# Performance work log

Measured on AMD Instinct MI355X. Metric: run time of the kernel, lower is better.

The kernel has to match this reference:

```python
import jax, jax.numpy as jnp
import numpy as np

CROP = 48
THRESHOLD = 0.5
IOU_THRESHOLD = 0.5


def _conv(x, w, b):
    # x: [N,H,W,C], w: [kh,kw,Cin,Cout]
    y = jax.lax.conv_general_dilated(x, w, (1, 1), 'VALID',
                                     dimension_numbers=('NHWC', 'HWIO', 'NHWC'))
    return y + b


def _prelu(x, a):
    # a broadcasts over the channel-last axis
    return jnp.where(x >= 0, x, a * x)


def _maxpool(x, k, s, p):
    return jax.lax.reduce_window(x, -jnp.inf, jax.lax.max,
                                 (1, k, k, 1), (1, s, s, 1),
                                 ((0, 0), (p, p), (p, p), (0, 0)))


def _nms_keep(boxes, scores, valid, iou_thr):
    # fixed-shape greedy NMS (torchvision semantics: suppress iou > thr)
    N = boxes.shape[0]
    s = jnp.where(valid, scores, -jnp.inf)
    order = jnp.argsort(-s)
    b = boxes[order]
    x1, y1, x2, y2 = b[:, 0], b[:, 1], b[:, 2], b[:, 3]
    area = (x2 - x1) * (y2 - y1)
    xx1 = jnp.maximum(x1[:, None], x1[None, :])
    yy1 = jnp.maximum(y1[:, None], y1[None, :])
    xx2 = jnp.minimum(x2[:, None], x2[None, :])
    yy2 = jnp.minimum(y2[:, None], y2[None, :])
    inter = jnp.clip(xx2 - xx1, 0.0) * jnp.clip(yy2 - yy1, 0.0)
    iou = inter / (area[:, None] + area[None, :] - inter + 1e-12)
    keep0 = valid[order]
    idx = jnp.arange(N)

    def body(i, keep):
        sup = (iou[i] > iou_thr) & (idx > i) & keep[i] & keep
        return keep & ~sup

    keep_sorted = jax.lax.fori_loop(0, N, body, keep0)
    return jnp.zeros(N, bool).at[order].set(keep_sorted)


def setup_inputs() -> dict:
    key = jax.random.key(0)
    ks = jax.random.split(key, 24)
    H = W = 1024
    N = 2048
    image = jax.random.uniform(ks[0], (H, W, 3), jnp.float32) * 255.0
    x1 = jax.random.uniform(ks[1], (N,), jnp.float32) * (W - 130)
    y1 = jax.random.uniform(ks[2], (N,), jnp.float32) * (H - 130)
    bw = 20.0 + jax.random.uniform(ks[3], (N,), jnp.float32) * 100.0
    bh = 20.0 + jax.random.uniform(ks[4], (N,), jnp.float32) * 100.0
    bboxes = jnp.stack([x1, y1, x1 + bw, y1 + bh], axis=1)
    rn = lambda k, sh, s: jax.random.normal(k, sh, jnp.float32) * s
    return {
        'bboxes': bboxes, 'image': image,
        'conv1_w': rn(ks[5], (3, 3, 3, 32), 0.05), 'conv1_b': rn(ks[6], (32,), 0.01),
        'prelu1': 0.25 * jnp.ones((32,), jnp.float32),
        'conv2_w': rn(ks[7], (3, 3, 32, 64), 0.05), 'conv2_b': rn(ks[8], (64,), 0.01),
        'prelu2': 0.25 * jnp.ones((64,), jnp.float32),
        'conv3_w': rn(ks[9], (3, 3, 64, 64), 0.05), 'conv3_b': rn(ks[10], (64,), 0.01),
        'prelu3': 0.25 * jnp.ones((64,), jnp.float32),
        'conv4_w': rn(ks[11], (2, 2, 64, 128), 0.05), 'conv4_b': rn(ks[12], (128,), 0.01),
        'prelu4': 0.25 * jnp.ones((128,), jnp.float32),
        'fc5_w': rn(ks[13], (256, 1152), 0.02), 'fc5_b': rn(ks[14], (256,), 0.01),
        'prelu5': 0.25 * jnp.ones((256,), jnp.float32),
        'fc6a_w': rn(ks[15], (2, 256), 0.1), 'fc6a_b': rn(ks[16], (2,), 0.01),
        'fc6b_w': rn(ks[17], (4, 256), 0.1), 'fc6b_b': rn(ks[18], (4,), 0.01),
    }


def reference(bboxes, image, conv1_w, conv1_b, prelu1, conv2_w, conv2_b, prelu2,
              conv3_w, conv3_b, prelu3, conv4_w, conv4_b, prelu4,
              fc5_w, fc5_b, prelu5, fc6a_w, fc6a_b, fc6b_w, fc6b_b):
    H, W = image.shape[0], image.shape[1]
    N = bboxes.shape[0]
    # preprocess (torch: (x - 127.5) * 0.0078125)
    data = (image - 127.5) * 0.0078125  # [H,W,3]
    # clip boxes in place like the torch forward
    bx1 = jnp.clip(bboxes[:, 0], 0.0, None)
    by1 = jnp.clip(bboxes[:, 1], 0.0, None)
    bx2 = jnp.clip(bboxes[:, 2], None, float(W))
    by2 = jnp.clip(bboxes[:, 3], None, float(H))
    bb = jnp.stack([bx1, by1, bx2, by2], axis=1)  # clipped boxes [N,4]
    # integer crop windows (torch .int() truncation; coords >= 0)
    ib = bb.astype(jnp.int32)
    cw = jnp.maximum(ib[:, 2] - ib[:, 0], 1)
    ch = jnp.maximum(ib[:, 3] - ib[:, 1], 1)
    # nearest-neighbor resize to 48x48 (F.interpolate default mode='nearest')
    r = jnp.arange(CROP, dtype=jnp.int32)
    xs = ib[:, 0:1] + (r[None, :] * cw[:, None]) // CROP  # [N,48]
    ys = ib[:, 1:2] + (r[None, :] * ch[:, None]) // CROP  # [N,48]
    crops = data[ys[:, :, None], xs[:, None, :], :]  # [N,48,48,3] gather
    # CNN trunk
    h = _maxpool(_prelu(_conv(crops, conv1_w, conv1_b), prelu1), 3, 2, 1)
    h = _maxpool(_prelu(_conv(h, conv2_w, conv2_b), prelu2), 3, 2, 0)
    h = _maxpool(_prelu(_conv(h, conv3_w, conv3_b), prelu3), 2, 2, 0)
    h = _prelu(_conv(h, conv4_w, conv4_b), prelu4)  # [N,3,3,128]
    h = jnp.transpose(h, (0, 3, 1, 2)).reshape(N, -1)  # NCHW flatten like torch -> [N,1152]
    h = _prelu(h @ fc5_w.T + fc5_b, prelu5)  # [N,256]
    cls = jax.nn.softmax(h @ fc6a_w.T + fc6a_b, axis=1)  # [N,2]
    reg = h @ fc6b_w.T + fc6b_b  # [N,4]
    score = cls[:, 1]
    valid = score >= THRESHOLD
    w = bb[:, 2] - bb[:, 0]
    hgt = bb[:, 3] - bb[:, 1]
    out = jnp.stack([bb[:, 0] + reg[:, 0] * w,
                     bb[:, 1] + reg[:, 1] * hgt,
                     bb[:, 2] + reg[:, 2] * w,
                     bb[:, 3] + reg[:, 3] * hgt], axis=1)  # [N,4]
    keep = _nms_keep(out, score, valid, IOU_THRESHOLD)
    return jnp.where(keep[:, None], out, 0.0)
```

## Files before the change

kernel.cpp:

```cpp
#include <hip/hip_runtime.h>
#include <math.h>
#include <stdint.h>

#define NBOX 2048

#define P1_RS 25
#define P1_CS 576
#define P1_SZ 18432

__device__ __forceinline__ void fma4(float4& a, float s, const float4& w) {
  a.x = fmaf(s, w.x, a.x); a.y = fmaf(s, w.y, a.y);
  a.z = fmaf(s, w.z, a.z); a.w = fmaf(s, w.w, a.w);
}
__device__ __forceinline__ float4 max4(float4 a, float4 b) {
  return make_float4(fmaxf(a.x,b.x), fmaxf(a.y,b.y), fmaxf(a.z,b.z), fmaxf(a.w,b.w));
}
__device__ __forceinline__ float4 max34(float4 a, float4 b, float4 c) {
  return max4(max4(a, b), c);
}
__device__ __forceinline__ float4 prelu4(float4 v, float4 a) {
  float4 r;
  r.x = v.x >= 0.f ? v.x : a.x*v.x;
  r.y = v.y >= 0.f ? v.y : a.y*v.y;
  r.z = v.z >= 0.f ? v.z : a.z*v.z;
  r.w = v.w >= 0.f ? v.w : a.w*v.w;
  return r;
}
__device__ __forceinline__ float4 shfl4(float4 v, int src) {
  float4 r;
  r.x = __shfl(v.x, src, 64); r.y = __shfl(v.y, src, 64);
  r.z = __shfl(v.z, src, 64); r.w = __shfl(v.w, src, 64);
  return r;
}

__global__ __launch_bounds__(256) void k1_crop_conv1(
    const float* __restrict__ bboxes, const float* __restrict__ image,
    const float* __restrict__ w1, const float* __restrict__ b1, const float* __restrict__ a1,
    float* __restrict__ p1ws, int box0)
{
  __shared__ float crop[48*48*3];
  __shared__ float w1s[27*32];
  __shared__ float b1s[32], a1s[32];
  const int tid = threadIdx.x;
  const int n = box0 + blockIdx.x;

  for (int idx = tid; idx < 27*32; idx += 256) w1s[idx] = w1[idx];
  if (tid < 32) { b1s[tid] = b1[tid]; a1s[tid] = a1[tid]; }

  float f0 = bboxes[n*4+0], f1 = bboxes[n*4+1], f2 = bboxes[n*4+2], f3 = bboxes[n*4+3];
  float bx1 = fmaxf(f0, 0.f), by1 = fmaxf(f1, 0.f);
  float bx2 = fminf(f2, 1024.f), by2 = fminf(f3, 1024.f);
  int ix1 = (int)bx1, iy1 = (int)by1, ix2 = (int)bx2, iy2 = (int)by2;
  int cw = ix2 - ix1; if (cw < 1) cw = 1;
  int ch = iy2 - iy1; if (ch < 1) ch = 1;

  for (int idx = tid; idx < 6912; idx += 256) {
    int c = idx % 3; int t = idx / 3; int j = t % 48; int i = t / 48;
    int gx = ix1 + (j * cw) / 48;
    int gy = iy1 + (i * ch) / 48;
    float v = image[(gy*1024 + gx)*3 + c];
    crop[idx] = (v - 127.5f) * 0.0078125f;
  }
  __syncthreads();

  float* p1o = p1ws + (size_t)blockIdx.x * P1_SZ;

  for (int slot = tid; slot < 1104; slot += 256) {
    int cq = slot & 7;
    int t2 = slot >> 3;
    int pjq = t2 % 6;
    int pi  = t2 / 6;
    int pj0 = pjq * 4;
    int c0 = 2*pj0 - 1;
    float4 bias  = *(const float4*)&b1s[cq*4];
    float4 alpha = *(const float4*)&a1s[cq*4];
    float4 mx[4];
#pragma unroll
    for (int t = 0; t < 4; t++) mx[t] = make_float4(-3.0e38f,-3.0e38f,-3.0e38f,-3.0e38f);

#pragma unroll
    for (int dr = 0; dr < 3; dr++) {
      int r = 2*pi - 1 + dr;
      if (r < 0 || r > 45) continue;
      float4 acc[9];
#pragma unroll
      for (int c = 0; c < 9; c++) acc[c] = bias;
#pragma unroll
      for (int kh = 0; kh < 3; kh++) {
        int row = r + kh;
        float s[33];
#pragma unroll
        for (int d = 0; d < 11; d++) {
          int cc = c0 + d; cc = cc < 0 ? 0 : (cc > 47 ? 47 : cc);
          int base = row*144 + cc*3;
          s[d*3+0] = crop[base+0];
          s[d*3+1] = crop[base+1];
          s[d*3+2] = crop[base+2];
        }
#pragma unroll
        for (int kw = 0; kw < 3; kw++) {
#pragma unroll
          for (int ci = 0; ci < 3; ci++) {
            float4 w = *(const float4*)&w1s[((kh*3+kw)*3+ci)*32 + cq*4];
#pragma unroll
            for (int c = 0; c < 9; c++) fma4(acc[c], s[(c+kw)*3+ci], w);
          }
        }
      }
#pragma unroll
      for (int c = 0; c < 9; c++) {
        int cabs = c0 + c;
        if (cabs < 0 || cabs > 45) continue;
        float4 pv = prelu4(acc[c], alpha);
#pragma unroll
        for (int t = 0; t < 4; t++) {
          if (c >= 2*t && c <= 2*t+2) mx[t] = max4(mx[t], pv);
        }
      }
    }
#pragma unroll
    for (int t = 0; t < 4; t++) {
      int pj = pj0 + t;
      if (pj < 23) {
        int base = pi*P1_RS + pj;
        p1o[(cq*4+0)*P1_CS + base] = mx[t].x;
        p1o[(cq*4+1)*P1_CS + base] = mx[t].y;
        p1o[(cq*4+2)*P1_CS + base] = mx[t].z;
        p1o[(cq*4+3)*P1_CS + base] = mx[t].w;
      }
    }
  }
}

#define K2_LOADW(W, CI, KH) { \
  const float* wp_ = w2 + (((KH)*3)*32 + (CI))*64 + co0; \
  W[0] = *(const float4*)(wp_);            W[1] = *(const float4*)(wp_ + 4); \
  W[2] = *(const float4*)(wp_ + 2048);     W[3] = *(const float4*)(wp_ + 2052); \
  W[4] = *(const float4*)(wp_ + 4096);     W[5] = *(const float4*)(wp_ + 4100); }

#define K2_COMP(W, CI, KH) { \
  const float* ip_ = &in_s[(CI)*P1_CS + (rl+(KH))*P1_RS + j0]; \
  float s_[9]; \
  _Pragma("unroll") for (int d_ = 0; d_ < 9; d_++) s_[d_] = ip_[d_]; \
  _Pragma("unroll") for (int kw_ = 0; kw_ < 3; kw_++) { \
    _Pragma("unroll") for (int jj_ = 0; jj_ < 7; jj_++) { \
      fma4(acc[jj_][0], s_[jj_+kw_], W[kw_*2]); \
      fma4(acc[jj_][1], s_[jj_+kw_], W[kw_*2+1]); } } }

#define K2_STORE8(PJ, LO, HI) { \
  float* d_ = p2o + (size_t)co0*120 + pi*12 + (PJ); \
  float4 lo_ = (LO), hi_ = (HI); \
  d_[0]   = lo_.x; d_[120] = lo_.y; d_[240] = lo_.z; d_[360] = lo_.w; \
  d_[480] = hi_.x; d_[600] = hi_.y; d_[720] = hi_.z; d_[840] = hi_.w; }

__global__ __launch_bounds__(512, 4) void k2_conv2(
    const float* __restrict__ w2, const float* __restrict__ b2, const float* __restrict__ a2,
    const float* __restrict__ p1ws, float* __restrict__ p2ws)
{
  __shared__ float in_s[P1_SZ];
  const int tid = threadIdx.x;
  const float* p1o = p1ws + (size_t)blockIdx.x * P1_SZ;
  float* p2o = p2ws + (size_t)blockIdx.x * 7680;

  for (int i4 = tid; i4 < P1_SZ/4; i4 += 512)
    *(float4*)&in_s[i4*4] = *(const float4*)&p1o[i4*4];
  __syncthreads();

  const int wav = __builtin_amdgcn_readfirstlane(tid >> 6);
  const int lane = tid & 63;
  int jt = lane / 21;
  int rl = lane - jt * 21;
  if (lane == 63) { jt = 2; rl = 20; }
  const int j0 = jt * 7;
  const int co0 = wav * 8;

  float4 bL = *(const float4*)&b2[co0];
  float4 bH = *(const float4*)&b2[co0+4];
  float4 aL = *(const float4*)&a2[co0];
  float4 aH = *(const float4*)&a2[co0+4];

  float4 acc[7][2];
#pragma unroll
  for (int jj = 0; jj < 7; jj++) { acc[jj][0] = bL; acc[jj][1] = bH; }

  float4 wA[6], wB[6];
  K2_LOADW(wA, 0, 0);
#pragma unroll 1
  for (int ci = 0; ci < 32; ci += 2) {
    K2_LOADW(wB, ci, 1);
    K2_COMP(wA, ci, 0);
    K2_LOADW(wA, ci, 2);
    K2_COMP(wB, ci, 1);
    K2_LOADW(wB, ci+1, 0);
    K2_COMP(wA, ci, 2);
    K2_LOADW(wA, ci+1, 1);
    K2_COMP(wB, ci+1, 0);
    K2_LOADW(wB, ci+1, 2);
    K2_COMP(wA, ci+1, 1);
    if (ci + 2 < 32) K2_LOADW(wA, ci+2, 0);
    K2_COMP(wB, ci+1, 2);
  }

#pragma unroll
  for (int jj = 0; jj < 7; jj++) {
    acc[jj][0] = prelu4(acc[jj][0], aL);
    acc[jj][1] = prelu4(acc[jj][1], aH);
  }

#pragma unroll
  for (int jj = 0; jj < 7; jj++) {
#pragma unroll
    for (int h = 0; h < 2; h++) {
      float4 v = acc[jj][h];
      float4 d1 = shfl4(v, lane + 1);
      float4 d2 = shfl4(v, lane + 2);
      acc[jj][h] = max34(v, d1, d2);
    }
  }
  float4 r0[2], r1[2];
#pragma unroll
  for (int h = 0; h < 2; h++) {
    r0[h] = shfl4(acc[0][h], lane + 21);
    r1[h] = shfl4(acc[1][h], lane + 21);
  }

  if (((rl & 1) == 0) && rl <= 18) {
    const int pi = rl >> 1;
    if (jt == 0) {
      K2_STORE8(0, max34(acc[0][0],acc[1][0],acc[2][0]), max34(acc[0][1],acc[1][1],acc[2][1]));
      K2_STORE8(1, max34(acc[2][0],acc[3][0],acc[4][0]), max34(acc[2][1],acc[3][1],acc[4][1]));
      K2_STORE8(2, max34(acc[4][0],acc[5][0],acc[6][0]), max34(acc[4][1],acc[5][1],acc[6][1]));
      K2_STORE8(3, max34(acc[6][0],r0[0],r1[0]),          max34(acc[6][1],r0[1],r1[1]));
    } else if (jt == 1) {
      K2_STORE8(4, max34(acc[1][0],acc[2][0],acc[3][0]), max34(acc[1][1],acc[2][1],acc[3][1]));
      K2_STORE8(5, max34(acc[3][0],acc[4][0],acc[5][0]), max34(acc[3][1],acc[4][1],acc[5][1]));
      K2_STORE8(6, max34(acc[5][0],acc[6][0],r0[0]),     max34(acc[5][1],acc[6][1],r0[1]));
    } else {
      K2_STORE8(7, max34(acc[0][0],acc[1][0],acc[2][0]), max34(acc[0][1],acc[1][1],acc[2][1]));
      K2_STORE8(8, max34(acc[2][0],acc[3][0],acc[4][0]), max34(acc[2][1],acc[3][1],acc[4][1]));
      K2_STORE8(9, max34(acc[4][0],acc[5][0],acc[6][0]), max34(acc[4][1],acc[5][1],acc[6][1]));
    }
  }
}

#define K3_LOADW(W, CI, KH) { \
  const float* wp_ = w3 + (((KH)*3)*64 + (CI))*64 + co0; \
  W[0] = *(const float4*)(wp_);            W[1] = *(const float4*)(wp_ + 4); \
  W[2] = *(const float4*)(wp_ + 4096);     W[3] = *(const float4*)(wp_ + 4100); \
  W[4] = *(const float4*)(wp_ + 8192);     W[5] = *(const float4*)(wp_ + 8196); }

#define K3_COMP(W, CI, KH) { \
  const float* ip_ = ibase + (CI)*120 + (KH)*12; \
  float2 sA_ = *(const float2*)(ip_); \
  float2 sB_ = *(const float2*)(ip_ + 2); \
  float s_[4] = {sA_.x, sA_.y, sB_.x, sB_.y}; \
  _Pragma("unroll") for (int kw_ = 0; kw_ < 3; kw_++) { \
    _Pragma("unroll") for (int c_ = 0; c_ < 2; c_++) { \
      fma4(acc[c_][0], s_[c_+kw_], W[kw_*2]); \
      fma4(acc[c_][1], s_[c_+kw_], W[kw_*2+1]); } } }

__global__ __launch_bounds__(512, 4) void k3_conv3(
    const float* __restrict__ w3, const float* __restrict__ b3, const float* __restrict__ a3,
    const float* __restrict__ p2ws, float* __restrict__ p3ws)
{
  __shared__ float in_s[15376];
  const int tid = threadIdx.x;
  const float* p2o = p2ws + (size_t)(blockIdx.x*2) * 7680;
  float* p3o0 = p3ws + (size_t)(blockIdx.x*2) * 1024;

  for (int i4 = tid; i4 < 3840; i4 += 512) {
    int bb = (i4 >= 1920) ? 1 : 0;
    int k = i4 - bb*1920;
    *(float4*)&in_s[bb*7688 + k*4] = *(const float4*)&p2o[(size_t)bb*7680 + k*4];
  }
  __syncthreads();

  const int wav = __builtin_amdgcn_readfirstlane(tid >> 6);
  const int lane = tid & 63;
  const int b  = lane >> 5;
  const int r  = (lane >> 2) & 7;
  const int cg = lane & 3;
  const int co0 = wav * 8;

  float4 bL = *(const float4*)&b3[co0];
  float4 bH = *(const float4*)&b3[co0+4];
  float4 aL = *(const float4*)&a3[co0];
  float4 aH = *(const float4*)&a3[co0+4];

  float4 acc[2][2];
  acc[0][0] = bL; acc[0][1] = bH; acc[1][0] = bL; acc[1][1] = bH;

  const float* ibase = &in_s[b*7688 + r*12 + cg*2];

  float4 wA[6], wB[6];
  K3_LOADW(wA, 0, 0);
#pragma unroll 1
  for (int ci = 0; ci < 64; ci += 2) {
    K3_LOADW(wB, ci, 1);
    K3_COMP(wA, ci, 0);
    K3_LOADW(wA, ci, 2);
    K3_COMP(wB, ci, 1);
    K3_LOADW(wB, ci+1, 0);
    K3_COMP(wA, ci, 2);
    K3_LOADW(wA, ci+1, 1);
    K3_COMP(wB, ci+1, 0);
    K3_LOADW(wB, ci+1, 2);
    K3_COMP(wA, ci+1, 1);
    if (ci + 2 < 64) K3_LOADW(wA, ci+2, 0);
    K3_COMP(wB, ci+1, 2);
  }

  float4 hm[2];
#pragma unroll
  for (int h = 0; h < 2; h++) {
    float4 p0 = prelu4(acc[0][h], h ? aH : aL);
    float4 p1 = prelu4(acc[1][h], h ? aH : aL);
    hm[h] = max4(p0, p1);
  }
  float4 o[2];
#pragma unroll
  for (int h = 0; h < 2; h++) {
    float4 d = shfl4(hm[h], lane + 4);
    o[h] = max4(hm[h], d);
  }
  if ((r & 1) == 0) {
    const int pi = r >> 1;
    float* d = p3o0 + b*1024 + (size_t)co0*16 + pi*4 + cg;
    d[0]   = o[0].x; d[16]  = o[0].y; d[32]  = o[0].z; d[48]  = o[0].w;
    d[64]  = o[1].x; d[80]  = o[1].y; d[96]  = o[1].z; d[112] = o[1].w;
  }
}

__global__ __launch_bounds__(128) void k4_conv4(
    const float* __restrict__ w4, const float* __restrict__ b4, const float* __restrict__ a4,
    const float* __restrict__ p3ws, float* __restrict__ c4ws)
{
  __shared__ float p3s[1024];
  __shared__ float w4s[64*128];
  __shared__ float b4s[128], a4s[128];
  const int tid = threadIdx.x;
  const float* p3o = p3ws + (size_t)blockIdx.x * 1024;
  float* c4o = c4ws + (size_t)blockIdx.x * 1152;
  b4s[tid] = b4[tid]; a4s[tid] = a4[tid];
  for (int idx4 = tid; idx4 < 256; idx4 += 128)
    *(float4*)&p3s[idx4*4] = *(const float4*)&p3o[idx4*4];

  const int slot = tid;
  const bool active = slot < 96;
  const int cq = slot & 31, rl = slot >> 5;
  float4 acc[3];
  bool first = true;
  for (int cg = 0; cg < 4; cg++) {
    __syncthreads();
    for (int idx4 = tid; idx4 < 2048; idx4 += 128) {
      int co4 = idx4 & 31, kkcl = idx4 >> 5;
      int khkw = kkcl >> 4, cl = kkcl & 15;
      *(float4*)&w4s[kkcl*128 + co4*4] =
          *(const float4*)&w4[(khkw*64 + cg*16 + cl)*128 + co4*4];
    }
    __syncthreads();
    if (active) {
      if (first) {
        float4 b = *(const float4*)&b4s[cq*4];
        acc[0]=b; acc[1]=b; acc[2]=b; first=false;
      }
      for (int cl = 0; cl < 16; cl++) {
        int ci = cg*16 + cl;
#pragma unroll
        for (int kh = 0; kh < 2; kh++) {
          float4 sv = *(const float4*)&p3s[ci*16 + (rl+kh)*4];
          float s[4] = {sv.x, sv.y, sv.z, sv.w};
#pragma unroll
          for (int kw = 0; kw < 2; kw++) {
            float4 w = *(const float4*)&w4s[((kh*2+kw)*16+cl)*128 + cq*4];
#pragma unroll
            for (int v = 0; v < 3; v++) fma4(acc[v], s[v+kw], w);
          }
        }
      }
    }
  }
  if (active) {
    float4 alpha = *(const float4*)&a4s[cq*4];
#pragma unroll
    for (int v = 0; v < 3; v++) {
      float4 p = prelu4(acc[v], alpha);
      c4o[(cq*4+0)*9 + rl*3 + v] = p.x;
      c4o[(cq*4+1)*9 + rl*3 + v] = p.y;
      c4o[(cq*4+2)*9 + rl*3 + v] = p.z;
      c4o[(cq*4+3)*9 + rl*3 + v] = p.w;
    }
  }
}

__global__ __launch_bounds__(256) void k5_fc(
    const float* __restrict__ fc5w, const float* __restrict__ fc5b, const float* __restrict__ a5,
    const float* __restrict__ w6a, const float* __restrict__ b6a,
    const float* __restrict__ w6b, const float* __restrict__ b6b,
    const float* __restrict__ bboxes, const float* __restrict__ c4ws,
    float* __restrict__ ws_scores, float* __restrict__ ws_boxes, int box0)
{
  __shared__ float c4s[8*1152];
  __shared__ float hs[8*256];
  __shared__ float l6[8][6];
  __shared__ float b5s[256], a5s[256];
  const int tid = threadIdx.x;
  const int lb0 = blockIdx.x * 8;
  b5s[tid] = fc5b[tid]; a5s[tid] = a5[tid];
  for (int idx4 = tid; idx4 < 2304; idx4 += 256)
    *(float4*)&c4s[idx4*4] = *(const float4*)&c4ws[(size_t)lb0*1152 + idx4*4];
  __syncthreads();

  const int og = tid & 31, bl = tid >> 5;
  float acc[8] = {0,0,0,0,0,0,0,0};
  const float* cbase = &c4s[bl*1152];
  for (int k = 0; k < 1152; k += 4) {
    float4 a = *(const float4*)&cbase[k];
#pragma unroll
    for (int u = 0; u < 8; u++) {
      int o = og + 32*u;
      float4 w = *(const float4*)&fc5w[(size_t)o*1152 + k];
      acc[u] += a.x*w.x + a.y*w.y + a.z*w.z + a.w*w.w;
    }
  }
#pragma unroll
  for (int u = 0; u < 8; u++) {
    int o = og + 32*u;
    float h = acc[u] + b5s[o];
    h = h >= 0.f ? h : a5s[o]*h;
    hs[bl*256 + o] = h;
  }
  __syncthreads();
  if (tid < 48) {
    int b = tid / 6, oi = tid % 6;
    const float* w = (oi < 2) ? &w6a[oi*256] : &w6b[(oi-2)*256];
    float d = (oi < 2) ? b6a[oi] : b6b[oi-2];
    const float* hh = &hs[b*256];
    for (int k = 0; k < 256; k++) d += hh[k]*w[k];
    l6[b][oi] = d;
  }
  __syncthreads();
  if (tid < 8) {
    int n = box0 + lb0 + tid;
    float l0 = l6[tid][0], l1 = l6[tid][1];
    float m = fmaxf(l0, l1);
    float e0 = expf(l0-m), e1 = expf(l1-m);
    float score = e1/(e0+e1);
    float r0 = l6[tid][2], r1 = l6[tid][3], r2 = l6[tid][4], r3 = l6[tid][5];
    float f0 = bboxes[n*4+0], f1 = bboxes[n*4+1], f2 = bboxes[n*4+2], f3 = bboxes[n*4+3];
    float bx1 = fmaxf(f0, 0.f), by1 = fmaxf(f1, 0.f);
    float bx2 = fminf(f2, 1024.f), by2 = fminf(f3, 1024.f);
    float w_ = bx2-bx1, h_ = by2-by1;
    ws_scores[n] = score;
    float4 ob = make_float4(bx1 + r0*w_, by1 + r1*h_, bx2 + r2*w_, by2 + r3*h_);
    *(float4*)&ws_boxes[n*4] = ob;
  }
}

__global__ __launch_bounds__(1024) void k6a_sort(
    const float* __restrict__ ws_scores, const float* __restrict__ ws_boxes,
    int* __restrict__ sidx_ws, float* __restrict__ sbox_ws,
    float* __restrict__ area_ws, int* __restrict__ nv_ws)
{
  __shared__ float skey[2048];
  __shared__ int   sidx[2048];
  const int tid = threadIdx.x;
  for (int i = tid; i < 2048; i += 1024) {
    float s = ws_scores[i];
    skey[i] = (s >= 0.5f) ? s : -INFINITY;
    sidx[i] = i;
  }
  __syncthreads();
  for (int k = 2; k <= 2048; k <<= 1) {
    for (int j = k >> 1; j > 0; j >>= 1) {
      for (int i = tid; i < 2048; i += 1024) {
        int ixj = i ^ j;
        if (ixj > i) {
          float a = skey[i], b = skey[ixj];
          int ia = sidx[i], ib = sidx[ixj];
          bool up = ((i & k) == 0);
          bool aAfterB = (a < b) || (a == b && ia > ib);
          if (up ? aAfterB : !aAfterB) {
            skey[i] = b; skey[ixj] = a; sidx[i] = ib; sidx[ixj] = ia;
          }
        }
      }
      __syncthreads();
    }
  }
  if (tid == 0) nv_ws[0] = 2048;
  __syncthreads();
  for (int i = tid; i < 2048; i += 1024) {
    if (skey[i] == -INFINITY && (i == 0 || skey[i-1] != -INFINITY)) nv_ws[0] = i;
    int n = sidx[i];
    sidx_ws[i] = n;
    float4 b = *(const float4*)&ws_boxes[n*4];
    *(float4*)&sbox_ws[i*4] = b;
    area_ws[i] = (b.z-b.x)*(b.w-b.y);
  }
}

__global__ __launch_bounds__(256) void k6b_iou(
    const int* __restrict__ nv_ws, const float* __restrict__ sbox_ws,
    const float* __restrict__ area_ws, unsigned long long* __restrict__ M)
{
  const int nv = nv_ws[0];
  int gt = blockIdx.x*256 + threadIdx.x;
  for (int w = gt; w < 2048*32; w += 128*256) {
    int i = w >> 5, wg = w & 31;
    if (i >= nv) continue;
    float4 bi = *(const float4*)&sbox_ws[i*4];
    float ai = area_ws[i];
    unsigned long long m = 0;
    int jbase = wg*64;
    if (jbase + 63 > i) {
      for (int jj = 0; jj < 64; jj++) {
        int j = jbase + jj;
        if (j <= i) continue;
        float4 bj = *(const float4*)&sbox_ws[j*4];
        float xx1 = fmaxf(bi.x, bj.x), yy1 = fmaxf(bi.y, bj.y);
        float xx2 = fminf(bi.z, bj.z), yy2 = fminf(bi.w, bj.w);
        float iw = fmaxf(xx2-xx1, 0.f), ih = fmaxf(yy2-yy1, 0.f);
        float inter = iw*ih;
        float iou = inter / (ai + area_ws[j] - inter + 1e-12f);
        if (iou > 0.5f) m |= (1ull << jj);
      }
    }
    M[w] = m;
  }
}

__global__ __launch_bounds__(1024) void k6c_scan(
    const int* __restrict__ nv_ws, const int* __restrict__ sidx_ws,
    const float* __restrict__ sbox_ws, const unsigned long long* __restrict__ M,
    float* __restrict__ out)
{
  __shared__ unsigned long long Msh[128*32];
  __shared__ unsigned long long rem_sh[32];
  const int tid = threadIdx.x;
  const int nv = nv_ws[0];
  unsigned long long rem = 0;

  for (int c0 = 0; c0 < 2048; c0 += 128) {
    if (c0 >= nv) break;
    for (int w = tid; w < 128*32; w += 1024) {
      int i = c0 + (w >> 5);
      if (i < nv) Msh[w] = M[(size_t)i*32 + (w & 31)];
    }
    __syncthreads();
    if (tid < 64) {
      int iend = c0 + 128; if (iend > nv) iend = nv;
      for (int i = c0; i < iend; i += 4) {
        unsigned long long m0=0, m1=0, m2=0, m3=0;
        int base = (i - c0) << 5;
        if (tid < 32) {
          m0 = Msh[base + tid];
          if (i+1 < iend) m1 = Msh[base + 32 + tid];
          if (i+2 < iend) m2 = Msh[base + 64 + tid];
          if (i+3 < iend) m3 = Msh[base + 96 + tid];
        }
        unsigned long long rw = __shfl(rem, (i >> 6), 64);
        if (!((rw >> (i & 63)) & 1ull)) rem |= m0;
        if (i+1 < iend) {
          rw = __shfl(rem, ((i+1) >> 6), 64);
          if (!((rw >> ((i+1) & 63)) & 1ull)) rem |= m1;
        }
        if (i+2 < iend) {
          rw = __shfl(rem, ((i+2) >> 6), 64);
          if (!((rw >> ((i+2) & 63)) & 1ull)) rem |= m2;
        }
        if (i+3 < iend) {
          rw = __shfl(rem, ((i+3) >> 6), 64);
          if (!((rw >> ((i+3) & 63)) & 1ull)) rem |= m3;
        }
      }
    }
    __syncthreads();
  }
  if (tid < 32) rem_sh[tid] = rem;
  __syncthreads();
  for (int i = tid; i < 2048; i += 1024) {
    bool keep = (i < nv) && !((rem_sh[i >> 6] >> (i & 63)) & 1ull);
    int n = sidx_ws[i];
    float4 b = *(const float4*)&sbox_ws[i*4];
    float4 o = keep ? b : make_float4(0.f,0.f,0.f,0.f);
    *(float4*)&out[n*4] = o;
  }
}

extern "C" void kernel_launch(void* const* d_in, const int* in_sizes, int n_in,
                              void* d_out, int out_size, void* d_ws, size_t ws_size,
                              hipStream_t stream)
{
  const float* bboxes = (const float*)d_in[0];
  const float* image  = (const float*)d_in[1];
  const float* w1 = (const float*)d_in[2];  const float* b1 = (const float*)d_in[3];  const float* a1 = (const float*)d_in[4];
  const float* w2 = (const float*)d_in[5];  const float* b2 = (const float*)d_in[6];  const float* a2 = (const float*)d_in[7];
  const float* w3 = (const float*)d_in[8];  const float* b3 = (const float*)d_in[9];  const float* a3 = (const float*)d_in[10];
  const float* w4 = (const float*)d_in[11]; const float* b4 = (const float*)d_in[12]; const float* a4 = (const float*)d_in[13];
  const float* fc5w = (const float*)d_in[14]; const float* fc5b = (const float*)d_in[15]; const float* a5 = (const float*)d_in[16];
  const float* w6a = (const float*)d_in[17]; const float* b6a = (const float*)d_in[18];
  const float* w6b = (const float*)d_in[19]; const float* b6b = (const float*)d_in[20];
  float* out = (float*)d_out;

  char* ws = (char*)d_ws;
  size_t off = 0;
  auto alloc = [&](size_t bytes) -> size_t {
    size_t p = off; off += (bytes + 255) & ~(size_t)255; return p;
  };
  size_t o_scores = alloc(NBOX*4);
  size_t o_boxes  = alloc(NBOX*16);
  size_t o_sidx   = alloc(NBOX*4);
  size_t o_sbox   = alloc(NBOX*16);
  size_t o_area   = alloc(NBOX*4);
  size_t o_nv     = alloc(256);
  size_t o_M      = alloc((size_t)NBOX*32*8);
  size_t fixed = off;
  const size_t perbox = (size_t)(P1_SZ + 7680 + 1024 + 1152) * 4;

  int B = NBOX;
  if (fixed + (size_t)B*perbox > ws_size) {
    size_t avail = ws_size > fixed ? ws_size - fixed : 0;
    B = (int)(avail / perbox);
    B &= ~7;
    if (B < 8) B = 8;
    if (B > NBOX) B = NBOX;
  }
  size_t o_p1 = alloc((size_t)B*P1_SZ*4);
  size_t o_p2 = alloc((size_t)B*7680*4);
  size_t o_p3 = alloc((size_t)B*1024*4);
  size_t o_c4 = alloc((size_t)B*1152*4);

  float* ws_scores = (float*)(ws + o_scores);
  float* ws_boxes  = (float*)(ws + o_boxes);
  int*   sidxp     = (int*)(ws + o_sidx);
  float* sboxp     = (float*)(ws + o_sbox);
  float* areap     = (float*)(ws + o_area);
  int*   nvp       = (int*)(ws + o_nv);
  unsigned long long* Mp = (unsigned long long*)(ws + o_M);
  float* p1p = (float*)(ws + o_p1);
  float* p2p = (float*)(ws + o_p2);
  float* p3p = (float*)(ws + o_p3);
  float* c4p = (float*)(ws + o_c4);

  for (int c0 = 0; c0 < NBOX; c0 += B) {
    int Bc = NBOX - c0; if (Bc > B) Bc = B;
    k1_crop_conv1<<<Bc, 256, 0, stream>>>(bboxes, image, w1, b1, a1, p1p, c0);
    k2_conv2<<<Bc, 512, 0, stream>>>(w2, b2, a2, p1p, p2p);
    k3_conv3<<<Bc/2, 512, 0, stream>>>(w3, b3, a3, p2p, p3p);
    k4_conv4<<<Bc, 128, 0, stream>>>(w4, b4, a4, p3p, c4p);
    k5_fc<<<Bc/8, 256, 0, stream>>>(fc5w, fc5b, a5, w6a, b6a, w6b, b6b,
                                    bboxes, c4p, ws_scores, ws_boxes, c0);
  }
  k6a_sort<<<1, 1024, 0, stream>>>(ws_scores, ws_boxes, sidxp, sboxp, areap, nvp);
  k6b_iou<<<128, 256, 0, stream>>>(nvp, sboxp, areap, Mp);
  k6c_scan<<<1, 1024, 0, stream>>>(nvp, sidxp, sboxp, Mp, out);
}
```

Baseline: 1.694 ms.

## Fuse crop, conv1-conv4 into one per-box kernel with LDS intermediates

Merges the separate crop+conv1, conv2, conv3 and conv4 kernels into a single 512-thread kernel per box. The intermediate activations now stay in shared memory instead of going through global workspace, and the chunked launch loop is removed. Conv3 and conv4 get new thread mappings (one box per block, single-accumulator conv3, direct global weight reads in conv4), and conv2 drops the double-buffered weight prefetch. The cost is about 110KB of LDS per block, which limits occupancy, and the light phases such as crop, conv3 and conv4 now leave many threads idle.

After: 2.460 ms. 1.45x slower.

```diff
diff --git a/kernel.cpp b/kernel.cpp
--- a/kernel.cpp
+++ b/kernel.cpp
@@ -7,6 +7,15 @@
 #define P1_RS 25
 #define P1_CS 576
 #define P1_SZ 18432
+
+#define OFF_P1   0
+#define OFF_CROP 18432
+#define OFF_P2   18432
+#define OFF_P3   (18432 + 7688)
+#define OFF_W1   (18432 + 8728)
+#define OFF_B1   (OFF_W1 + 864)
+#define OFF_A1   (OFF_B1 + 32)
+#define SMEM_FLOATS 28088
 
 __device__ __forceinline__ void fma4(float4& a, float s, const float4& w) {
   a.x = fmaf(s, w.x, a.x); a.y = fmaf(s, w.y, a.y);
@@ -33,18 +42,55 @@
   return r;
 }
 
-__global__ __launch_bounds__(256) void k1_crop_conv1(
+#define K2_LOADW(W, CI, KH) { \
+  const float* wp_ = w2 + (((KH)*3)*32 + (CI))*64 + co0; \
+  W[0] = *(const float4*)(wp_);            W[1] = *(const float4*)(wp_ + 4); \
+  W[2] = *(const float4*)(wp_ + 2048);     W[3] = *(const float4*)(wp_ + 2052); \
+  W[4] = *(const float4*)(wp_ + 4096);     W[5] = *(const float4*)(wp_ + 4100); }
+
+#define K2_COMP(W, CI, KH) { \
+  const float* ip_ = &p1s[(CI)*P1_CS + (rl+(KH))*P1_RS + j0]; \
+  float s_[9]; \
+  _Pragma("unroll") for (int d_ = 0; d_ < 9; d_++) s_[d_] = ip_[d_]; \
+  _Pragma("unroll") for (int kw_ = 0; kw_ < 3; kw_++) { \
+    _Pragma("unroll") for (int jj_ = 0; jj_ < 7; jj_++) { \
+      fma4(acc[jj_][0], s_[jj_+kw_], W[kw_*2]); \
+      fma4(acc[jj_][1], s_[jj_+kw_], W[kw_*2+1]); } } }
+
+#define K2_STORE8(PJ, LO, HI) { \
+  float* d_ = p2s + co0*120 + pi*12 + (PJ); \
+  float4 lo_ = (LO), hi_ = (HI); \
+  d_[0]   = lo_.x; d_[120] = lo_.y; d_[240] = lo_.z; d_[360] = lo_.w; \
+  d_[480] = hi_.x; d_[600] = hi_.y; d_[720] = hi_.z; d_[840] = hi_.w; }
+
+#define K3_LOADW(W, CI, KH) { \
+  const float* wp_ = w3 + (((KH)*3)*64 + (CI))*64 + co0; \
+  W[0] = *(const float4*)(wp_);            W[1] = *(const float4*)(wp_ + 4); \
+  W[2] = *(const float4*)(wp_ + 4096);     W[3] = *(const float4*)(wp_ + 4100); \
+  W[4] = *(const float4*)(wp_ + 8192);     W[5] = *(const float4*)(wp_ + 8196); }
+
+__global__ __launch_bounds__(512) void k_fused(
     const float* __restrict__ bboxes, const float* __restrict__ image,
     const float* __restrict__ w1, const float* __restrict__ b1, const float* __restrict__ a1,
-    float* __restrict__ p1ws, int box0)
+    const float* __restrict__ w2, const float* __restrict__ b2, const float* __restrict__ a2,
+    const float* __restrict__ w3, const float* __restrict__ b3, const float* __restrict__ a3,
+    const float* __restrict__ w4, const float* __restrict__ b4, const float* __restrict__ a4,
+    float* __restrict__ c4ws)
 {
-  __shared__ float crop[48*48*3];
-  __shared__ float w1s[27*32];
-  __shared__ float b1s[32], a1s[32];
+  __shared__ float smem[SMEM_FLOATS];
+  float* p1s  = smem + OFF_P1;
+  float* crop = smem + OFF_CROP;
+  float* p2s  = smem + OFF_P2;
+  float* p3s  = smem + OFF_P3;
+  float* w1s  = smem + OFF_W1;
+  float* b1s  = smem + OFF_B1;
+  float* a1s  = smem + OFF_A1;
   const int tid = threadIdx.x;
-  const int n = box0 + blockIdx.x;
-
-  for (int idx = tid; idx < 27*32; idx += 256) w1s[idx] = w1[idx];
+  const int n = blockIdx.x;
+  const int wav = __builtin_amdgcn_readfirstlane(tid >> 6);
+  const int lane = tid & 63;
+
+  for (int idx = tid; idx < 864; idx += 512) w1s[idx] = w1[idx];
   if (tid < 32) { b1s[tid] = b1[tid]; a1s[tid] = a1[tid]; }
 
   float f0 = bboxes[n*4+0], f1 = bboxes[n*4+1], f2 = bboxes[n*4+2], f3 = bboxes[n*4+3];
@@ -53,8 +99,7 @@
   int ix1 = (int)bx1, iy1 = (int)by1, ix2 = (int)bx2, iy2 = (int)by2;
   int cw = ix2 - ix1; if (cw < 1) cw = 1;
   int ch = iy2 - iy1; if (ch < 1) ch = 1;
-
-  for (int idx = tid; idx < 6912; idx += 256) {
+  for (int idx = tid; idx < 6912; idx += 512) {
     int c = idx % 3; int t = idx / 3; int j = t % 48; int i = t / 48;
     int gx = ix1 + (j * cw) / 48;
     int gy = iy1 + (i * ch) / 48;
@@ -63,9 +108,7 @@
   }
   __syncthreads();
 
-  float* p1o = p1ws + (size_t)blockIdx.x * P1_SZ;
-
-  for (int slot = tid; slot < 1104; slot += 256) {
+  for (int slot = tid; slot < 1104; slot += 512) {
     int cq = slot & 7;
     int t2 = slot >> 3;
     int pjq = t2 % 6;
@@ -123,272 +166,151 @@
       int pj = pj0 + t;
       if (pj < 23) {
         int base = pi*P1_RS + pj;
-        p1o[(cq*4+0)*P1_CS + base] = mx[t].x;
-        p1o[(cq*4+1)*P1_CS + base] = mx[t].y;
-        p1o[(cq*4+2)*P1_CS + base] = mx[t].z;
-        p1o[(cq*4+3)*P1_CS + base] = mx[t].w;
-      }
-    }
-  }
-}
-
-#define K2_LOADW(W, CI, KH) { \
-  const float* wp_ = w2 + (((KH)*3)*32 + (CI))*64 + co0; \
-  W[0] = *(const float4*)(wp_);            W[1] = *(const float4*)(wp_ + 4); \
-  W[2] = *(const float4*)(wp_ + 2048);     W[3] = *(const float4*)(wp_ + 2052); \
-  W[4] = *(const float4*)(wp_ + 4096);     W[5] = *(const float4*)(wp_ + 4100); }
-
-#define K2_COMP(W, CI, KH) { \
-  const float* ip_ = &in_s[(CI)*P1_CS + (rl+(KH))*P1_RS + j0]; \
-  float s_[9]; \
-  _Pragma("unroll") for (int d_ = 0; d_ < 9; d_++) s_[d_] = ip_[d_]; \
-  _Pragma("unroll") for (int kw_ = 0; kw_ < 3; kw_++) { \
-    _Pragma("unroll") for (int jj_ = 0; jj_ < 7; jj_++) { \
-      fma4(acc[jj_][0], s_[jj_+kw_], W[kw_*2]); \
-      fma4(acc[jj_][1], s_[jj_+kw_], W[kw_*2+1]); } } }
-
-#define K2_STORE8(PJ, LO, HI) { \
-  float* d_ = p2o + (size_t)co0*120 + pi*12 + (PJ); \
-  float4 lo_ = (LO), hi_ = (HI); \
-  d_[0]   = lo_.x; d_[120] = lo_.y; d_[240] = lo_.z; d_[360] = lo_.w; \
-  d_[480] = hi_.x; d_[600] = hi_.y; d_[720] = hi_.z; d_[840] = hi_.w; }
-
-__global__ __launch_bounds__(512, 4) void k2_conv2(
-    const float* __restrict__ w2, const float* __restrict__ b2, const float* __restrict__ a2,
-    const float* __restrict__ p1ws, float* __restrict__ p2ws)
-{
-  __shared__ float in_s[P1_SZ];
-  const int tid = threadIdx.x;
-  const float* p1o = p1ws + (size_t)blockIdx.x * P1_SZ;
-  float* p2o = p2ws + (size_t)blockIdx.x * 7680;
-
-  for (int i4 = tid; i4 < P1_SZ/4; i4 += 512)
-    *(float4*)&in_s[i4*4] = *(const float4*)&p1o[i4*4];
-  __syncthreads();
-
-  const int wav = __builtin_amdgcn_readfirstlane(tid >> 6);
-  const int lane = tid & 63;
-  int jt = lane / 21;
-  int rl = lane - jt * 21;
-  if (lane == 63) { jt = 2; rl = 20; }
-  const int j0 = jt * 7;
-  const int co0 = wav * 8;
-
-  float4 bL = *(const float4*)&b2[co0];
-  float4 bH = *(const float4*)&b2[co0+4];
-  float4 aL = *(const float4*)&a2[co0];
-  float4 aH = *(const float4*)&a2[co0+4];
-
-  float4 acc[7][2];
-#pragma unroll
-  for (int jj = 0; jj < 7; jj++) { acc[jj][0] = bL; acc[jj][1] = bH; }
-
-  float4 wA[6], wB[6];
-  K2_LOADW(wA, 0, 0);
+        p1s[(cq*4+0)*P1_CS + base] = mx[t].x;
+        p1s[(cq*4+1)*P1_CS + base] = mx[t].y;
+        p1s[(cq*4+2)*P1_CS + base] = mx[t].z;
+        p1s[(cq*4+3)*P1_CS + base] = mx[t].w;
+      }
+    }
+  }
+  __syncthreads();
+
+  {
+    int jt = lane / 21;
+    int rl = lane - jt * 21;
+    if (lane == 63) { jt = 2; rl = 20; }
+    const int j0 = jt * 7;
+    const int co0 = wav * 8;
+
+    float4 bL = *(const float4*)&b2[co0];
+    float4 bH = *(const float4*)&b2[co0+4];
+    float4 aL = *(const float4*)&a2[co0];
+    float4 aH = *(const float4*)&a2[co0+4];
+
+    float4 acc[7][2];
+#pragma unroll
+    for (int jj = 0; jj < 7; jj++) { acc[jj][0] = bL; acc[jj][1] = bH; }
+
 #pragma unroll 1
-  for (int ci = 0; ci < 32; ci += 2) {
-    K2_LOADW(wB, ci, 1);
-    K2_COMP(wA, ci, 0);
-    K2_LOADW(wA, ci, 2);
-    K2_COMP(wB, ci, 1);
-    K2_LOADW(wB, ci+1, 0);
-    K2_COMP(wA, ci, 2);
-    K2_LOADW(wA, ci+1, 1);
-    K2_COMP(wB, ci+1, 0);
-    K2_LOADW(wB, ci+1, 2);
-    K2_COMP(wA, ci+1, 1);
-    if (ci + 2 < 32) K2_LOADW(wA, ci+2, 0);
-    K2_COMP(wB, ci+1, 2);
-  }
-
-#pragma unroll
-  for (int jj = 0; jj < 7; jj++) {
-    acc[jj][0] = prelu4(acc[jj][0], aL);
-    acc[jj][1] = prelu4(acc[jj][1], aH);
-  }
-
-#pragma unroll
-  for (int jj = 0; jj < 7; jj++) {
+    for (int ci = 0; ci < 32; ci++) {
+      float4 q0[6], q1[6], q2[6];
+      K2_LOADW(q0, ci, 0);
+      K2_LOADW(q1, ci, 1);
+      K2_COMP(q0, ci, 0);
+      K2_LOADW(q2, ci, 2);
+      K2_COMP(q1, ci, 1);
+      K2_COMP(q2, ci, 2);
+    }
+
+#pragma unroll
+    for (int jj = 0; jj < 7; jj++) {
+      acc[jj][0] = prelu4(acc[jj][0], aL);
+      acc[jj][1] = prelu4(acc[jj][1], aH);
+    }
+#pragma unroll
+    for (int jj = 0; jj < 7; jj++) {
+#pragma unroll
+      for (int h = 0; h < 2; h++) {
+        float4 v = acc[jj][h];
+        float4 d1 = shfl4(v, lane + 1);
+        float4 d2 = shfl4(v, lane + 2);
+        acc[jj][h] = max34(v, d1, d2);
+      }
+    }
+    float4 r0[2], r1[2];
 #pragma unroll
     for (int h = 0; h < 2; h++) {
-      float4 v = acc[jj][h];
-      float4 d1 = shfl4(v, lane + 1);
-      float4 d2 = shfl4(v, lane + 2);
-      acc[jj][h] = max34(v, d1, d2);
-    }
-  }
-  float4 r0[2], r1[2];
-#pragma unroll
-  for (int h = 0; h < 2; h++) {
-    r0[h] = shfl4(acc[0][h], lane + 21);
-    r1[h] = shfl4(acc[1][h], lane + 21);
-  }
-
-  if (((rl & 1) == 0) && rl <= 18) {
-    const int pi = rl >> 1;
-    if (jt == 0) {
-      K2_STORE8(0, max34(acc[0][0],acc[1][0],acc[2][0]), max34(acc[0][1],acc[1][1],acc[2][1]));
-      K2_STORE8(1, max34(acc[2][0],acc[3][0],acc[4][0]), max34(acc[2][1],acc[3][1],acc[4][1]));
-      K2_STORE8(2, max34(acc[4][0],acc[5][0],acc[6][0]), max34(acc[4][1],acc[5][1],acc[6][1]));
-      K2_STORE8(3, max34(acc[6][0],r0[0],r1[0]),          max34(acc[6][1],r0[1],r1[1]));
-    } else if (jt == 1) {
-      K2_STORE8(4, max34(acc[1][0],acc[2][0],acc[3][0]), max34(acc[1][1],acc[2][1],acc[3][1]));
-      K2_STORE8(5, max34(acc[3][0],acc[4][0],acc[5][0]), max34(acc[3][1],acc[4][1],acc[5][1]));
-      K2_STORE8(6, max34(acc[5][0],acc[6][0],r0[0]),     max34(acc[5][1],acc[6][1],r0[1]));
-    } else {
-      K2_STORE8(7, max34(acc[0][0],acc[1][0],acc[2][0]), max34(acc[0][1],acc[1][1],acc[2][1]));
-      K2_STORE8(8, max34(acc[2][0],acc[3][0],acc[4][0]), max34(acc[2][1],acc[3][1],acc[4][1]));
-      K2_STORE8(9, max34(acc[4][0],acc[5][0],acc[6][0]), max34(acc[4][1],acc[5][1],acc[6][1]));
-    }
-  }
-}
-
-#define K3_LOADW(W, CI, KH) { \
-  const float* wp_ = w3 + (((KH)*3)*64 + (CI))*64 + co0; \
-  W[0] = *(const float4*)(wp_);            W[1] = *(const float4*)(wp_ + 4); \
-  W[2] = *(const float4*)(wp_ + 4096);     W[3] = *(const float4*)(wp_ + 4100); \
-  W[4] = *(const float4*)(wp_ + 8192);     W[5] = *(const float4*)(wp_ + 8196); }
-
-#define K3_COMP(W, CI, KH) { \
-  const float* ip_ = ibase + (CI)*120 + (KH)*12; \
-  float2 sA_ = *(const float2*)(ip_); \
-  float2 sB_ = *(const float2*)(ip_ + 2); \
-  float s_[4] = {sA_.x, sA_.y, sB_.x, sB_.y}; \
-  _Pragma("unroll") for (int kw_ = 0; kw_ < 3; kw_++) { \
-    _Pragma("unroll") for (int c_ = 0; c_ < 2; c_++) { \
-      fma4(acc[c_][0], s_[c_+kw_], W[kw_*2]); \
-      fma4(acc[c_][1], s_[c_+kw_], W[kw_*2+1]); } } }
-
-__global__ __launch_bounds__(512, 4) void k3_conv3(
-    const float* __restrict__ w3, const float* __restrict__ b3, const float* __restrict__ a3,
-    const float* __restrict__ p2ws, float* __restrict__ p3ws)
-{
-  __shared__ float in_s[15376];
-  const int tid = threadIdx.x;
-  const float* p2o = p2ws + (size_t)(blockIdx.x*2) * 7680;
-  float* p3o0 = p3ws + (size_t)(blockIdx.x*2) * 1024;
-
-  for (int i4 = tid; i4 < 3840; i4 += 512) {
-    int bb = (i4 >= 1920) ? 1 : 0;
-    int k = i4 - bb*1920;
-    *(float4*)&in_s[bb*7688 + k*4] = *(const float4*)&p2o[(size_t)bb*7680 + k*4];
-  }
-  __syncthreads();
-
-  const int wav = __builtin_amdgcn_readfirstlane(tid >> 6);
-  const int lane = tid & 63;
-  const int b  = lane >> 5;
-  const int r  = (lane >> 2) & 7;
-  const int cg = lane & 3;
-  const int co0 = wav * 8;
-
-  float4 bL = *(const float4*)&b3[co0];
-  float4 bH = *(const float4*)&b3[co0+4];
-  float4 aL = *(const float4*)&a3[co0];
-  float4 aH = *(const float4*)&a3[co0+4];
-
-  float4 acc[2][2];
-  acc[0][0] = bL; acc[0][1] = bH; acc[1][0] = bL; acc[1][1] = bH;
-
-  const float* ibase = &in_s[b*7688 + r*12 + cg*2];
-
-  float4 wA[6], wB[6];
-  K3_LOADW(wA, 0, 0);
+      r0[h] = shfl4(acc[0][h], lane + 21);
+      r1[h] = shfl4(acc[1][h], lane + 21);
+    }
+
+    if (((rl & 1) == 0) && rl <= 18) {
+      const int pi = rl >> 1;
+      if (jt == 0) {
+        K2_STORE8(0, max34(acc[0][0],acc[1][0],acc[2][0]), max34(acc[0][1],acc[1][1],acc[2][1]));
+        K2_STORE8(1, max34(acc[2][0],acc[3][0],acc[4][0]), max34(acc[2][1],acc[3][1],acc[4][1]));
+        K2_STORE8(2, max34(acc[4][0],acc[5][0],acc[6][0]), max34(acc[4][1],acc[5][1],acc[6][1]));
+        K2_STORE8(3, max34(acc[6][0],r0[0],r1[0]),          max34(acc[6][1],r0[1],r1[1]));
+      } else if (jt == 1) {
+        K2_STORE8(4, max34(acc[1][0],acc[2][0],acc[3][0]), max34(acc[1][1],acc[2][1],acc[3][1]));
+        K2_STORE8(5, max34(acc[3][0],acc[4][0],acc[5][0]), max34(acc[3][1],acc[4][1],acc[5][1]));
+        K2_STORE8(6, max34(acc[5][0],acc[6][0],r0[0]),     max34(acc[5][1],acc[6][1],r0[1]));
+      } else {
+        K2_STORE8(7, max34(acc[0][0],acc[1][0],acc[2][0]), max34(acc[0][1],acc[1][1],acc[2][1]));
+        K2_STORE8(8, max34(acc[2][0],acc[3][0],acc[4][0]), max34(acc[2][1],acc[3][1],acc[4][1]));
+        K2_STORE8(9, max34(acc[4][0],acc[5][0],acc[6][0]), max34(acc[4][1],acc[5][1],acc[6][1]));
+      }
+    }
+  }
+  __syncthreads();
+
+  {
+    const int r3 = lane >> 3;
+    const int jc = lane & 7;
+    const int co0 = wav * 8;
+
+    float4 bL = *(const float4*)&b3[co0];
+    float4 bH = *(const float4*)&b3[co0+4];
+    float4 aL = *(const float4*)&a3[co0];
+    float4 aH = *(const float4*)&a3[co0+4];
+    float4 a0 = bL, a1v = bH;
+
 #pragma unroll 1
-  for (int ci = 0; ci < 64; ci += 2) {
-    K3_LOADW(wB, ci, 1);
-    K3_COMP(wA, ci, 0);
-    K3_LOADW(wA, ci, 2);
-    K3_COMP(wB, ci, 1);
-    K3_LOADW(wB, ci+1, 0);
-    K3_COMP(wA, ci, 2);
-    K3_LOADW(wA, ci+1, 1);
-    K3_COMP(wB, ci+1, 0);
-    K3_LOADW(wB, ci+1, 2);
-    K3_COMP(wA, ci+1, 1);
-    if (ci + 2 < 64) K3_LOADW(wA, ci+2, 0);
-    K3_COMP(wB, ci+1, 2);
-  }
-
-  float4 hm[2];
-#pragma unroll
-  for (int h = 0; h < 2; h++) {
-    float4 p0 = prelu4(acc[0][h], h ? aH : aL);
-    float4 p1 = prelu4(acc[1][h], h ? aH : aL);
-    hm[h] = max4(p0, p1);
-  }
-  float4 o[2];
-#pragma unroll
-  for (int h = 0; h < 2; h++) {
-    float4 d = shfl4(hm[h], lane + 4);
-    o[h] = max4(hm[h], d);
-  }
-  if ((r & 1) == 0) {
-    const int pi = r >> 1;
-    float* d = p3o0 + b*1024 + (size_t)co0*16 + pi*4 + cg;
-    d[0]   = o[0].x; d[16]  = o[0].y; d[32]  = o[0].z; d[48]  = o[0].w;
-    d[64]  = o[1].x; d[80]  = o[1].y; d[96]  = o[1].z; d[112] = o[1].w;
-  }
-}
-
-__global__ __launch_bounds__(128) void k4_conv4(
-    const float* __restrict__ w4, const float* __restrict__ b4, const float* __restrict__ a4,
-    const float* __restrict__ p3ws, float* __restrict__ c4ws)
-{
-  __shared__ float p3s[1024];
-  __shared__ float w4s[64*128];
-  __shared__ float b4s[128], a4s[128];
-  const int tid = threadIdx.x;
-  const float* p3o = p3ws + (size_t)blockIdx.x * 1024;
-  float* c4o = c4ws + (size_t)blockIdx.x * 1152;
-  b4s[tid] = b4[tid]; a4s[tid] = a4[tid];
-  for (int idx4 = tid; idx4 < 256; idx4 += 128)
-    *(float4*)&p3s[idx4*4] = *(const float4*)&p3o[idx4*4];
-
-  const int slot = tid;
-  const bool active = slot < 96;
-  const int cq = slot & 31, rl = slot >> 5;
-  float4 acc[3];
-  bool first = true;
-  for (int cg = 0; cg < 4; cg++) {
-    __syncthreads();
-    for (int idx4 = tid; idx4 < 2048; idx4 += 128) {
-      int co4 = idx4 & 31, kkcl = idx4 >> 5;
-      int khkw = kkcl >> 4, cl = kkcl & 15;
-      *(float4*)&w4s[kkcl*128 + co4*4] =
-          *(const float4*)&w4[(khkw*64 + cg*16 + cl)*128 + co4*4];
-    }
-    __syncthreads();
-    if (active) {
-      if (first) {
-        float4 b = *(const float4*)&b4s[cq*4];
-        acc[0]=b; acc[1]=b; acc[2]=b; first=false;
-      }
-      for (int cl = 0; cl < 16; cl++) {
-        int ci = cg*16 + cl;
-#pragma unroll
-        for (int kh = 0; kh < 2; kh++) {
-          float4 sv = *(const float4*)&p3s[ci*16 + (rl+kh)*4];
-          float s[4] = {sv.x, sv.y, sv.z, sv.w};
-#pragma unroll
-          for (int kw = 0; kw < 2; kw++) {
-            float4 w = *(const float4*)&w4s[((kh*2+kw)*16+cl)*128 + cq*4];
-#pragma unroll
-            for (int v = 0; v < 3; v++) fma4(acc[v], s[v+kw], w);
-          }
-        }
-      }
-    }
-  }
-  if (active) {
-    float4 alpha = *(const float4*)&a4s[cq*4];
-#pragma unroll
-    for (int v = 0; v < 3; v++) {
-      float4 p = prelu4(acc[v], alpha);
-      c4o[(cq*4+0)*9 + rl*3 + v] = p.x;
-      c4o[(cq*4+1)*9 + rl*3 + v] = p.y;
-      c4o[(cq*4+2)*9 + rl*3 + v] = p.z;
-      c4o[(cq*4+3)*9 + rl*3 + v] = p.w;
+    for (int ci = 0; ci < 64; ci++) {
+      float4 W0[6], W1[6], W2[6];
+      K3_LOADW(W0, ci, 0);
+      K3_LOADW(W1, ci, 1);
+      K3_LOADW(W2, ci, 2);
+      const float* ip0 = p2s + ci*120 + r3*12 + jc;
+      float s0[3], s1[3], s2[3];
+#pragma unroll
+      for (int d = 0; d < 3; d++) { s0[d] = ip0[d]; s1[d] = ip0[12+d]; s2[d] = ip0[24+d]; }
+#pragma unroll
+      for (int kw = 0; kw < 3; kw++) {
+        fma4(a0, s0[kw], W0[kw*2]); fma4(a1v, s0[kw], W0[kw*2+1]);
+        fma4(a0, s1[kw], W1[kw*2]); fma4(a1v, s1[kw], W1[kw*2+1]);
+        fma4(a0, s2[kw], W2[kw*2]); fma4(a1v, s2[kw], W2[kw*2+1]);
+      }
+    }
+    a0  = prelu4(a0,  aL);
+    a1v = prelu4(a1v, aH);
+    float4 h0 = max4(a0,  shfl4(a0,  lane + 1));
+    float4 h1 = max4(a1v, shfl4(a1v, lane + 1));
+    float4 o0 = max4(h0, shfl4(h0, lane + 8));
+    float4 o1 = max4(h1, shfl4(h1, lane + 8));
+    if (((r3 & 1) == 0) && ((jc & 1) == 0)) {
+      float* d = p3s + co0*16 + (r3 >> 1)*4 + (jc >> 1);
+      d[0]  = o0.x; d[16] = o0.y; d[32] = o0.z; d[48]  = o0.w;
+      d[64] = o1.x; d[80] = o1.y; d[96] = o1.z; d[112] = o1.w;
+    }
+  }
+  __syncthreads();
+
+  {
+    const int coq = lane >> 4;
+    const int sp  = lane & 15;
+    const bool act = sp < 9;
+    const int sq = act ? sp : 8;
+    const int r4 = sq / 3, cc4 = sq - 3*r4;
+    const int co4 = wav*16 + coq*4;
+    float4 acc4 = *(const float4*)&b4[co4];
+#pragma unroll 1
+    for (int ci = 0; ci < 64; ci++) {
+      const float* ip = p3s + ci*16 + r4*4 + cc4;
+      float i00 = ip[0], i01 = ip[1], i10 = ip[4], i11 = ip[5];
+      const float* wp = w4 + ci*128 + co4;
+      float4 W00 = *(const float4*)(wp);
+      float4 W01 = *(const float4*)(wp + 8192);
+      float4 W10 = *(const float4*)(wp + 16384);
+      float4 W11 = *(const float4*)(wp + 24576);
+      fma4(acc4, i00, W00); fma4(acc4, i01, W01);
+      fma4(acc4, i10, W10); fma4(acc4, i11, W11);
+    }
+    if (act) {
+      float4 al = *(const float4*)&a4[co4];
+      float4 p = prelu4(acc4, al);
+      float* d = c4ws + (size_t)n*1152 + (size_t)co4*9 + sp;
+      d[0] = p.x; d[9] = p.y; d[18] = p.z; d[27] = p.w;
     }
   }
 }
@@ -398,7 +320,7 @@
     const float* __restrict__ w6a, const float* __restrict__ b6a,
     const float* __restrict__ w6b, const float* __restrict__ b6b,
     const float* __restrict__ bboxes, const float* __restrict__ c4ws,
-    float* __restrict__ ws_scores, float* __restrict__ ws_boxes, int box0)
+    float* __restrict__ ws_scores, float* __restrict__ ws_boxes)
 {
   __shared__ float c4s[8*1152];
   __shared__ float hs[8*256];
@@ -441,7 +363,7 @@
   }
   __syncthreads();
   if (tid < 8) {
-    int n = box0 + lb0 + tid;
+    int n = lb0 + tid;
     float l0 = l6[tid][0], l1 = l6[tid][1];
     float m = fmaxf(l0, l1);
     float e0 = expf(l0-m), e1 = expf(l1-m);
@@ -615,21 +537,7 @@
   size_t o_area   = alloc(NBOX*4);
   size_t o_nv     = alloc(256);
   size_t o_M      = alloc((size_t)NBOX*32*8);
-  size_t fixed = off;
-  const size_t perbox = (size_t)(P1_SZ + 7680 + 1024 + 1152) * 4;
-
-  int B = NBOX;
-  if (fixed + (size_t)B*perbox > ws_size) {
-    size_t avail = ws_size > fixed ? ws_size - fixed : 0;
-    B = (int)(avail / perbox);
-    B &= ~7;
-    if (B < 8) B = 8;
-    if (B > NBOX) B = NBOX;
-  }
-  size_t o_p1 = alloc((size_t)B*P1_SZ*4);
-  size_t o_p2 = alloc((size_t)B*7680*4);
-  size_t o_p3 = alloc((size_t)B*1024*4);
-  size_t o_c4 = alloc((size_t)B*1152*4);
+  size_t o_c4     = alloc((size_t)NBOX*1152*4);
 
   float* ws_scores = (float*)(ws + o_scores);
   float* ws_boxes  = (float*)(ws + o_boxes);
@@ -638,20 +546,12 @@
   float* areap     = (float*)(ws + o_area);
   int*   nvp       = (int*)(ws + o_nv);
   unsigned long long* Mp = (unsigned long long*)(ws + o_M);
-  float* p1p = (float*)(ws + o_p1);
-  float* p2p = (float*)(ws + o_p2);
-  float* p3p = (float*)(ws + o_p3);
   float* c4p = (float*)(ws + o_c4);
 
-  for (int c0 = 0; c0 < NBOX; c0 += B) {
-    int Bc = NBOX - c0; if (Bc > B) Bc = B;
-    k1_crop_conv1<<<Bc, 256, 0, stream>>>(bboxes, image, w1, b1, a1, p1p, c0);
-    k2_conv2<<<Bc, 512, 0, stream>>>(w2, b2, a2, p1p, p2p);
-    k3_conv3<<<Bc/2, 512, 0, stream>>>(w3, b3, a3, p2p, p3p);
-    k4_conv4<<<Bc, 128, 0, stream>>>(w4, b4, a4, p3p, c4p);
-    k5_fc<<<Bc/8, 256, 0, stream>>>(fc5w, fc5b, a5, w6a, b6a, w6b, b6b,
-                                    bboxes, c4p, ws_scores, ws_boxes, c0);
-  }
+  k_fused<<<NBOX, 512, 0, stream>>>(bboxes, image, w1, b1, a1, w2, b2, a2,
+                                    w3, b3, a3, w4, b4, a4, c4p);
+  k5_fc<<<NBOX/8, 256, 0, stream>>>(fc5w, fc5b, a5, w6a, b6a, w6b, b6b,
+                                    bboxes, c4p, ws_scores, ws_boxes);
   k6a_sort<<<1, 1024, 0, stream>>>(ws_scores, ws_boxes, sidxp, sboxp, areap, nvp);
   k6b_iou<<<128, 256, 0, stream>>>(nvp, sboxp, areap, Mp);
   k6c_scan<<<1, 1024, 0, stream>>>(nvp, sidxp, sboxp, Mp, out);
```
